# Optimization experiments

Hardware: AMD Instinct MI355X
Metric: run time of the kernel (lower is better)

## Reference

```python
import jax, jax.numpy as jnp
import numpy as np

K = 9
STRIDE = 1
UNFOLDINGS = 12
N_SIGMA = 1
SIGMA_MIN, SIGMA_MAX = 0.0, 50.0


def soft_threshold(x, lmbda):
    return jnp.sign(x) * jnp.maximum(jnp.abs(x) - lmbda, 0.0)


def lookup_arr(value):
    # arr = [sigma_min + d*i for i in range(n_sigma+1)], d=(max-min)/n_sigma
    d = (SIGMA_MAX - SIGMA_MIN) / N_SIGMA
    arr = [SIGMA_MIN + d * i for i in range(N_SIGMA + 1)]
    for i, x in enumerate(arr):
        if value <= x:
            return max(i - 1, 0)
    return len(arr) - 2


def im2col(I, k, s):
    # torch F.unfold ordering: channel-major, then kh, kw -> [B, C*k*k, Ho, Wo]
    B, C, H, W = I.shape
    Ho = (H - k) // s + 1
    Wo = (W - k) // s + 1
    cols = jnp.stack(
        [I[:, :, i:i + (Ho - 1) * s + 1:s, j:j + (Wo - 1) * s + 1:s]
         for i in range(k) for j in range(k)], axis=2)  # [B, C, k*k, Ho, Wo]
    return cols.reshape(B, C * k * k, Ho, Wo)


def col2im_avg(cols, H, W, k, s):
    # F.fold with averaging by overlap counts
    B, Ckk, Ho, Wo = cols.shape
    C = Ckk // (k * k)
    x = cols.reshape(B, C, k, k, Ho, Wo)
    out = jnp.zeros((B, C, H, W), cols.dtype)
    cnt = jnp.zeros((1, 1, H, W), cols.dtype)
    one = jnp.ones((1, 1, Ho, Wo), cols.dtype)
    for i in range(k):
        for j in range(k):
            sl_h = slice(i, i + (Ho - 1) * s + 1, s)
            sl_w = slice(j, j + (Wo - 1) * s + 1, s)
            out = out.at[:, :, sl_h, sl_w].add(x[:, :, i, j])
            cnt = cnt.at[:, :, sl_h, sl_w].add(one)
    return out / cnt


def setup_inputs() -> dict:
    key = jax.random.key(0)
    k1, k2 = jax.random.split(key)
    Ckk = K * K * 3  # 243
    F = 256
    I = jax.random.normal(k1, (4, 3, 128, 128), dtype=jnp.float32)
    # Dictionary init normalized by sqrt of top singular value ~ spectral norm
    D = jax.random.normal(k2, (Ckk, F), dtype=jnp.float32)
    s_max = jnp.linalg.norm(D.T @ D, ord=2)
    D = D / jnp.sqrt(s_max)
    A = D.T                      # [F, Ckk]
    Dw = jnp.array(D)            # [Ckk, F]
    Ww = jnp.array(D)            # [Ckk, F]
    lmbdas = jnp.full((UNFOLDINGS, F), 0.01, dtype=jnp.float32)
    return {"I": I, "A": A, "Dw": Dw, "Ww": Ww, "lmbdas": lmbdas, "sigma_hat": 25}


def reference(I, A, Dw, Ww, lmbdas, sigma_hat):
    noise_set = lookup_arr(sigma_hat)  # python int, trace-time constant
    B, C, H, W = I.shape
    I_col = im2col(I, K, STRIDE)                     # [B, Ckk, Ho, Wo]
    mean_patch = I_col.mean(axis=1, keepdims=True)   # centered patches
    I_c = I_col - mean_patch
    lin = jnp.einsum('fc,bchw->bfhw', A, I_c)
    lm = lmbdas[noise_set * UNFOLDINGS][None, :, None, None]
    gamma = soft_threshold(lin, lm)
    for kk in range(UNFOLDINGS - 1):
        x_k = jnp.einsum('cf,bfhw->bchw', Dw, gamma)
        r_k = jnp.einsum('fc,bchw->bfhw', A, x_k - I_c)
        lm = lmbdas[noise_set * UNFOLDINGS + kk + 1][None, :, None, None]
        gamma = soft_threshold(gamma - r_k, lm)
    out_all = jnp.einsum('cf,bfhw->bchw', Ww, gamma) + mean_patch
    return col2im_avg(out_all, H, W, K, STRIDE)
```

## Files before the change

### kernel.cpp

```cpp
#include <hip/hip_runtime.h>
#include <stdint.h>

typedef __attribute__((ext_vector_type(8))) short bf16x8;
typedef __attribute__((ext_vector_type(4))) float f32x4;

__device__ __forceinline__ unsigned short f2bf(float f) {
  union { float f; unsigned u; } v; v.f = f;
  unsigned u = v.u;
  u += 0x7fffu + ((u >> 16) & 1u);
  return (unsigned short)(u >> 16);
}
__device__ __forceinline__ float bfpk_lo(unsigned pk) {
  union { unsigned u; float f; } v; v.u = pk << 16; return v.f;
}
__device__ __forceinline__ float bfpk_hi(unsigned pk) {
  union { unsigned u; float f; } v; v.u = pk & 0xffff0000u; return v.f;
}

__device__ __forceinline__ int swz_idx(int k, int n) {
  return ((((k >> 5) * 16 + (n >> 4)) * 64) + (((k >> 3) & 3) * 16 + (n & 15))) * 8 + (k & 7);
}

#define ST_STRIDE 272

__device__ __attribute__((aligned(16))) unsigned short g_Acswz[65536];
__device__ __attribute__((aligned(16))) unsigned short g_Gswz[65536];
__device__ __attribute__((aligned(16))) unsigned short g_W3swz[65536];

__global__ void prep_all(const float* __restrict__ A, const float* __restrict__ Dw,
                         const float* __restrict__ Ww, float* __restrict__ out) {
  __shared__ float red[256];
  const int b = blockIdx.x;
  const int tid = threadIdx.x;
  out[b * 256 + tid] = 0.f;

  if (b < 256) {
    float s = 0.f;
    for (int c = tid; c < 243; c += 256) s += A[b * 243 + c];
    red[tid] = s;
    __syncthreads();
    for (int off = 128; off; off >>= 1) {
      if (tid < off) red[tid] += red[tid + off];
      __syncthreads();
    }
    float rm = red[0] * (1.f / 243.f);
    int k = tid;
    float v = 0.f;
    if (k < 243) {
      int rw = k / 9, j = k - rw * 9;
      int i = rw / 3, c = rw - i * 3;
      int corig = c * 81 + i * 9 + j;
      v = A[b * 243 + corig] - rm;
    }
    g_Acswz[swz_idx(k, b)] = f2bf(v);
  } else if (b < 512) {
    int f = b - 256, fp = tid;
    const float* Ar = A + f * 243;
    float s0 = 0.f, s1 = 0.f, s2 = 0.f, s3 = 0.f;
    int c = 0;
    for (; c + 4 <= 240; c += 4) {
      s0 += Ar[c + 0] * Dw[(c + 0) * 256 + fp];
      s1 += Ar[c + 1] * Dw[(c + 1) * 256 + fp];
      s2 += Ar[c + 2] * Dw[(c + 2) * 256 + fp];
      s3 += Ar[c + 3] * Dw[(c + 3) * 256 + fp];
    }
    s0 += Ar[240] * Dw[240 * 256 + fp];
    s1 += Ar[241] * Dw[241 * 256 + fp];
    s2 += Ar[242] * Dw[242 * 256 + fp];
    float s = (s0 + s1) + (s2 + s3);
    g_Gswz[swz_idx(fp, f)] = f2bf(((f == fp) ? 1.f : 0.f) - s);
  } else {
    int cc = b - 512, f = tid;
    float v = 0.f;
    if (cc < 243) {
      int rw = cc / 9, j = cc - rw * 9;
      int i = rw / 3, c = rw - i * 3;
      int corig = c * 81 + i * 9 + j;
      v = Ww[corig * 256 + f];
    }
    g_W3swz[swz_idx(f, cc)] = f2bf(v);
  }
}

template <int CMODE>
__device__ __forceinline__ void run_gemm(const unsigned short* __restrict__ Bsrc,
                                         const unsigned short* stg, int w, int lane,
                                         int m, int q, f32x4 (&acc)[4][4],
                                         const unsigned (&linpk)[4][4][2]) {
  bf16x8 bb[3][4];
#pragma unroll
  for (int p = 0; p < 2; ++p)
#pragma unroll
    for (int un = 0; un < 4; ++un)
      bb[p][un] = *(const bf16x8*)(Bsrc + (((p * 16 + 4 * w + un) * 64 + lane) << 3));
#pragma unroll
  for (int s = 0; s < 8; ++s) {
    if (s < 6) {
#pragma unroll
      for (int un = 0; un < 4; ++un)
        bb[(s + 2) % 3][un] =
            *(const bf16x8*)(Bsrc + ((((s + 2) * 16 + 4 * w + un) * 64 + lane) << 3));
    }
#pragma unroll
    for (int t = 0; t < 4; ++t) {
      bf16x8 afr = *(const bf16x8*)(stg + (t * 16 + m) * ST_STRIDE + s * 32 + q * 8);
#pragma unroll
      for (int un = 0; un < 4; ++un) {
        f32x4 cin;
        if (s == 0) {
          if (CMODE == 1) {
            cin[0] = bfpk_lo(linpk[t][un][0]);
            cin[1] = bfpk_hi(linpk[t][un][0]);
            cin[2] = bfpk_lo(linpk[t][un][1]);
            cin[3] = bfpk_hi(linpk[t][un][1]);
          } else {
            cin = (f32x4){0.f, 0.f, 0.f, 0.f};
          }
        } else {
          cin = acc[t][un];
        }
        acc[t][un] = __builtin_amdgcn_mfma_f32_16x16x32_bf16(afr, bb[s % 3][un], cin, 0, 0, 0);
      }
    }
  }
}

__global__ __launch_bounds__(256, 2) void lista_fused(
    const float* __restrict__ I, const float* __restrict__ lmb, float* __restrict__ out) {
  __shared__ __attribute__((aligned(16))) unsigned short stage[2][64 * ST_STRIDE];
  __shared__ float img[3][16][16];
  __shared__ float meanv[64];
  __shared__ float outacc[768];

  const int tid = threadIdx.x;
  const int lane = tid & 63;
  const int w = tid >> 6;
  const int m = lane & 15;
  const int q = lane >> 4;

  const int blk = blockIdx.x;
  const int b = blk / 225;
  const int t2 = blk - b * 225;
  const int ty = t2 / 15;
  const int tx = t2 - ty * 15;
  const int py0 = ty * 8, px0 = tx * 8;

  const float* Ib = I + b * (3 * 128 * 128);
  for (int r = tid; r < 768; r += 256) {
    int c = r >> 8;
    int yx = r & 255;
    int y = yx >> 4, x = yx & 15;
    img[c][y][x] = Ib[c * 16384 + (py0 + y) * 128 + (px0 + x)];
    outacc[r] = 0.f;
  }
  if (tid < 64) meanv[tid] = 0.f;
  __syncthreads();

  {
    const int pos = tid & 63;
    const int part = tid >> 6;
    const int y = pos >> 3, x = pos & 7;
    int j = part, c = 0, i = 0;
    float s = 0.f;
    unsigned short* srow = &stage[0][pos * ST_STRIDE];
    for (int kk = 0; kk < 64; ++kk) {
      int k = part + 4 * kk;
      float v = 0.f;
      if (k < 243) { v = img[c][y + i][x + j]; s += v; }
      srow[k] = f2bf(v);
      j += 4;
      if (j >= 9) { j -= 9; if (++c == 3) { c = 0; ++i; } }
    }
    atomicAdd(&meanv[pos], s * (1.f / 243.f));
  }
  __syncthreads();

  f32x4 acc[4][4];
  unsigned linpk[4][4][2];

  run_gemm<0>(g_Acswz, stage[0], w, lane, m, q, acc, linpk);

#pragma unroll
  for (int un = 0; un < 4; ++un) {
    int f = 64 * w + un * 16 + m;
    float lam = lmb[f];
#pragma unroll
    for (int t = 0; t < 4; ++t) {
      linpk[t][un][0] = (unsigned)f2bf(acc[t][un][0]) | ((unsigned)f2bf(acc[t][un][1]) << 16);
      linpk[t][un][1] = (unsigned)f2bf(acc[t][un][2]) | ((unsigned)f2bf(acc[t][un][3]) << 16);
#pragma unroll
      for (int r = 0; r < 4; ++r) {
        float x0 = acc[t][un][r];
        float g = x0 - fminf(fmaxf(x0, -lam), lam);
        stage[1][(t * 16 + q * 4 + r) * ST_STRIDE + f] = f2bf(g);
      }
    }
  }
  __syncthreads();

  for (int kk = 0; kk < 11; ++kk) {
    const int rb = (kk & 1) ^ 1;
    run_gemm<1>(g_Gswz, stage[rb], w, lane, m, q, acc, linpk);
#pragma unroll
    for (int un = 0; un < 4; ++un) {
      int f = 64 * w + un * 16 + m;
      float lam = lmb[(kk + 1) * 256 + f];
#pragma unroll
      for (int t = 0; t < 4; ++t)
#pragma unroll
        for (int r = 0; r < 4; ++r) {
          float x0 = acc[t][un][r];
          float g = x0 - fminf(fmaxf(x0, -lam), lam);
          stage[rb ^ 1][(t * 16 + q * 4 + r) * ST_STRIDE + f] = f2bf(g);
        }
    }
    __syncthreads();
  }

  run_gemm<0>(g_W3swz, stage[0], w, lane, m, q, acc, linpk);

#pragma unroll
  for (int un = 0; un < 4; ++un) {
    int cc = 64 * w + un * 16 + m;
    if (cc < 243) {
      int rw = cc / 9, jj = cc - rw * 9;
      int i = rw / 3, c = rw - i * 3;
#pragma unroll
      for (int t = 0; t < 4; ++t)
#pragma unroll
        for (int r = 0; r < 4; ++r) {
          int pos = t * 16 + q * 4 + r;
          int y = (pos >> 3) + i, x = (pos & 7) + jj;
          float val = acc[t][un][r] + meanv[pos];
          atomicAdd(&outacc[c * 256 + y * 16 + x], val);
        }
    }
  }
  __syncthreads();

  float* Ob = out + b * (3 * 128 * 128);
  for (int r = tid; r < 768; r += 256) {
    int c = r >> 8;
    int yx = r & 255;
    int y = yx >> 4, x = yx & 15;
    atomicAdd(&Ob[c * 16384 + (py0 + y) * 128 + (px0 + x)], outacc[r]);
  }
}

__global__ void div_counts(float* __restrict__ out, int n) {
  int idx = blockIdx.x * 256 + threadIdx.x;
  if (idx >= n) return;
  int x = idx & 127, y = (idx >> 7) & 127;
  int loy = y - 8; if (loy < 0) loy = 0;
  int hiy = y; if (hiy > 119) hiy = 119;
  int lox = x - 8; if (lox < 0) lox = 0;
  int hix = x; if (hix > 119) hix = 119;
  float cnt = (float)((hiy - loy + 1) * (hix - lox + 1));
  out[idx] = out[idx] / cnt;
}

extern "C" void kernel_launch(void* const* d_in, const int* in_sizes, int n_in,
                              void* d_out, int out_size, void* d_ws, size_t ws_size,
                              hipStream_t stream) {
  const float* I = (const float*)d_in[0];
  const float* A = (const float*)d_in[1];
  const float* Dw = (const float*)d_in[2];
  const float* Ww = (const float*)d_in[3];
  const float* lmb = (const float*)d_in[4];
  float* out = (float*)d_out;
  (void)d_ws; (void)ws_size;

  prep_all<<<768, 256, 0, stream>>>(A, Dw, Ww, out);
  lista_fused<<<900, 256, 0, stream>>>(I, lmb, out);
  div_counts<<<768, 256, 0, stream>>>(out, out_size);
}
```

Before: 291.6 us.

## Move lin accumulator to LDS and single-buffer stage to cut registers

```diff
diff --git a/kernel.cpp b/kernel.cpp
--- a/kernel.cpp
+++ b/kernel.cpp
@@ -3,6 +3,7 @@
 
 typedef __attribute__((ext_vector_type(8))) short bf16x8;
 typedef __attribute__((ext_vector_type(4))) float f32x4;
+typedef __attribute__((ext_vector_type(2))) unsigned u32x2;
 
 __device__ __forceinline__ unsigned short f2bf(float f) {
   union { float f; unsigned u; } v; v.f = f;
@@ -86,7 +87,7 @@
 __device__ __forceinline__ void run_gemm(const unsigned short* __restrict__ Bsrc,
                                          const unsigned short* stg, int w, int lane,
                                          int m, int q, f32x4 (&acc)[4][4],
-                                         const unsigned (&linpk)[4][4][2]) {
+                                         const unsigned* __restrict__ linw) {
   bf16x8 bb[3][4];
 #pragma unroll
   for (int p = 0; p < 2; ++p)
@@ -109,10 +110,11 @@
         f32x4 cin;
         if (s == 0) {
           if (CMODE == 1) {
-            cin[0] = bfpk_lo(linpk[t][un][0]);
-            cin[1] = bfpk_hi(linpk[t][un][0]);
-            cin[2] = bfpk_lo(linpk[t][un][1]);
-            cin[3] = bfpk_hi(linpk[t][un][1]);
+            u32x2 lp = *(const u32x2*)(linw + (t * 4 + un) * 128);
+            cin[0] = bfpk_lo(lp[0]);
+            cin[1] = bfpk_hi(lp[0]);
+            cin[2] = bfpk_lo(lp[1]);
+            cin[3] = bfpk_hi(lp[1]);
           } else {
             cin = (f32x4){0.f, 0.f, 0.f, 0.f};
           }
@@ -127,10 +129,10 @@
 
 __global__ __launch_bounds__(256, 2) void lista_fused(
     const float* __restrict__ I, const float* __restrict__ lmb, float* __restrict__ out) {
-  __shared__ __attribute__((aligned(16))) unsigned short stage[2][64 * ST_STRIDE];
-  __shared__ float img[3][16][16];
+  __shared__ __attribute__((aligned(16))) unsigned short stage[64 * ST_STRIDE];
+  __shared__ __attribute__((aligned(16))) unsigned linld[8192];
+  __shared__ __attribute__((aligned(16))) float ibuf[768];
   __shared__ float meanv[64];
-  __shared__ float outacc[768];
 
   const int tid = threadIdx.x;
   const int lane = tid & 63;
@@ -145,13 +147,14 @@
   const int tx = t2 - ty * 15;
   const int py0 = ty * 8, px0 = tx * 8;
 
+  unsigned* linw = linld + w * 2048 + lane * 2;
+
   const float* Ib = I + b * (3 * 128 * 128);
   for (int r = tid; r < 768; r += 256) {
     int c = r >> 8;
     int yx = r & 255;
     int y = yx >> 4, x = yx & 15;
-    img[c][y][x] = Ib[c * 16384 + (py0 + y) * 128 + (px0 + x)];
-    outacc[r] = 0.f;
+    ibuf[r] = Ib[c * 16384 + (py0 + y) * 128 + (px0 + x)];
   }
   if (tid < 64) meanv[tid] = 0.f;
   __syncthreads();
@@ -162,11 +165,11 @@
     const int y = pos >> 3, x = pos & 7;
     int j = part, c = 0, i = 0;
     float s = 0.f;
-    unsigned short* srow = &stage[0][pos * ST_STRIDE];
+    unsigned short* srow = &stage[pos * ST_STRIDE];
     for (int kk = 0; kk < 64; ++kk) {
       int k = part + 4 * kk;
       float v = 0.f;
-      if (k < 243) { v = img[c][y + i][x + j]; s += v; }
+      if (k < 243) { v = ibuf[c * 256 + (y + i) * 16 + (x + j)]; s += v; }
       srow[k] = f2bf(v);
       j += 4;
       if (j >= 9) { j -= 9; if (++c == 3) { c = 0; ++i; } }
@@ -175,10 +178,12 @@
   }
   __syncthreads();
 
+  for (int r = tid; r < 768; r += 256) ibuf[r] = 0.f;
+
   f32x4 acc[4][4];
-  unsigned linpk[4][4][2];
-
-  run_gemm<0>(g_Acswz, stage[0], w, lane, m, q, acc, linpk);
+
+  run_gemm<0>(g_Acswz, stage, w, lane, m, q, acc, nullptr);
+  __syncthreads();
 
 #pragma unroll
   for (int un = 0; un < 4; ++un) {
@@ -186,21 +191,22 @@
     float lam = lmb[f];
 #pragma unroll
     for (int t = 0; t < 4; ++t) {
-      linpk[t][un][0] = (unsigned)f2bf(acc[t][un][0]) | ((unsigned)f2bf(acc[t][un][1]) << 16);
-      linpk[t][un][1] = (unsigned)f2bf(acc[t][un][2]) | ((unsigned)f2bf(acc[t][un][3]) << 16);
+      unsigned l0 = (unsigned)f2bf(acc[t][un][0]) | ((unsigned)f2bf(acc[t][un][1]) << 16);
+      unsigned l1 = (unsigned)f2bf(acc[t][un][2]) | ((unsigned)f2bf(acc[t][un][3]) << 16);
+      *(u32x2*)(linw + (t * 4 + un) * 128) = (u32x2){l0, l1};
 #pragma unroll
       for (int r = 0; r < 4; ++r) {
         float x0 = acc[t][un][r];
         float g = x0 - fminf(fmaxf(x0, -lam), lam);
-        stage[1][(t * 16 + q * 4 + r) * ST_STRIDE + f] = f2bf(g);
+        stage[(t * 16 + q * 4 + r) * ST_STRIDE + f] = f2bf(g);
       }
     }
   }
   __syncthreads();
 
   for (int kk = 0; kk < 11; ++kk) {
-    const int rb = (kk & 1) ^ 1;
-    run_gemm<1>(g_Gswz, stage[rb], w, lane, m, q, acc, linpk);
+    run_gemm<1>(g_Gswz, stage, w, lane, m, q, acc, linw);
+    __syncthreads();
 #pragma unroll
     for (int un = 0; un < 4; ++un) {
       int f = 64 * w + un * 16 + m;
@@ -211,13 +217,13 @@
         for (int r = 0; r < 4; ++r) {
           float x0 = acc[t][un][r];
           float g = x0 - fminf(fmaxf(x0, -lam), lam);
-          stage[rb ^ 1][(t * 16 + q * 4 + r) * ST_STRIDE + f] = f2bf(g);
+          stage[(t * 16 + q * 4 + r) * ST_STRIDE + f] = f2bf(g);
         }
     }
     __syncthreads();
   }
 
-  run_gemm<0>(g_W3swz, stage[0], w, lane, m, q, acc, linpk);
+  run_gemm<0>(g_W3swz, stage, w, lane, m, q, acc, nullptr);
 
 #pragma unroll
   for (int un = 0; un < 4; ++un) {
@@ -232,7 +238,7 @@
           int pos = t * 16 + q * 4 + r;
           int y = (pos >> 3) + i, x = (pos & 7) + jj;
           float val = acc[t][un][r] + meanv[pos];
-          atomicAdd(&outacc[c * 256 + y * 16 + x], val);
+          atomicAdd(&ibuf[c * 256 + y * 16 + x], val);
         }
     }
   }
@@ -243,7 +249,7 @@
     int c = r >> 8;
     int yx = r & 255;
     int y = yx >> 4, x = yx & 15;
-    atomicAdd(&Ob[c * 16384 + (py0 + y) * 128 + (px0 + x)], outacc[r]);
+    atomicAdd(&Ob[c * 16384 + (py0 + y) * 128 + (px0 + x)], ibuf[r]);
   }
 }
 
```

New measurement: 280.2 us. 1.04x faster.
